# Performance work log

Measured on AMD Instinct MI355X. Metric: run time of the kernel, lower is better.

Reference implementation:

```python
import jax, jax.numpy as jnp
import numpy as np

B, L, E, H = 2, 2048, 1024, 16
HD = E // H


def _rel_shift(x):
    # x: [b, h, q, k] -> Transformer-XL relative shift via pad+reshape trick
    b, h, q, k = x.shape
    xp = jnp.pad(x, ((0, 0), (0, 0), (0, 0), (1, 0)))  # pad left of last dim
    xp = xp.reshape(b, h, k + 1, q)
    return xp[:, :, 1:, :].reshape(b, h, q, k)


def setup_inputs() -> dict:
    key = jax.random.key(0)
    ks = jax.random.split(key, 16)
    s = 0.02
    return {
        "query": jax.random.normal(ks[0], (B, L, E), jnp.float32),
        "key": jax.random.normal(ks[1], (B, L, E), jnp.float32),
        "value": jax.random.normal(ks[2], (B, L, E), jnp.float32),
        "pos_embedding": jax.random.normal(ks[3], (B, L, E), jnp.float32),
        "Wq": jax.random.normal(ks[4], (E, E), jnp.float32) * s,
        "bq": jnp.zeros((E,), jnp.float32),
        "Wk": jax.random.normal(ks[5], (E, E), jnp.float32) * s,
        "bk": jnp.zeros((E,), jnp.float32),
        "Wv": jax.random.normal(ks[6], (E, E), jnp.float32) * s,
        "bv": jnp.zeros((E,), jnp.float32),
        "Wp": jax.random.normal(ks[7], (E, E), jnp.float32) * s,  # Pos linear, no bias
        "Wo": jax.random.normal(ks[8], (E, E), jnp.float32) * s,
        "bo": jnp.zeros((E,), jnp.float32),
        "U": jax.random.normal(ks[9], (H, HD), jnp.float32) * s,
        "V": jax.random.normal(ks[10], (H, HD), jnp.float32) * s,
    }


def reference(query, key, value, pos_embedding, Wq, bq, Wk, bk, Wv, bv, Wp, Wo, bo, U, V):
    b, qlen, e = query.shape
    h, hd = U.shape
    scale = jnp.sqrt(jnp.asarray(e, query.dtype))
    # torch Linear: y = x @ W.T + b
    q = (query @ Wq.T + bq).reshape(b, qlen, h, hd)
    k = (key @ Wk.T + bk).reshape(b, key.shape[1], h, hd)
    v = (value @ Wv.T + bv).reshape(b, value.shape[1], h, hd)
    r = (pos_embedding @ Wp.T).reshape(b, -1, h, hd)
    content_score = jnp.einsum("bqhd,bkhd->bhqk", q + U, k)
    position_score = jnp.einsum("bqhd,bkhd->bhqk", q + V, r)
    position_score = _rel_shift(position_score)
    attention_score = (content_score + position_score) / scale
    # NOTE: the original module applies NO softmax; faithful reproduction.
    # einsum 'bhqk,bvhd->bqhd' sums over both k (scores) and v (values).
    alpha = jnp.einsum("bhqk,bvhd->bqhd", attention_score, v).reshape(b, qlen, e)
    return alpha @ Wo.T + bo
```

## Files before the change

### kernel.cpp

```cpp
#include <hip/hip_runtime.h>

#define BB 2
#define LL 2048
#define EE 1024
#define HH 16
#define HDD 64

typedef __bf16 bf16x8 __attribute__((ext_vector_type(8)));
typedef float f32x4 __attribute__((ext_vector_type(4)));

__device__ __forceinline__ unsigned short f2bf(float f) {
  unsigned int x = __float_as_uint(f);
  return (unsigned short)((x + 0x7FFFu + ((x >> 16) & 1u)) >> 16);
}

__global__ __launch_bounds__(256) void cast_kernel(
    const float* __restrict__ q, const float* __restrict__ pe,
    const float* __restrict__ wq, const float* __restrict__ wp,
    unsigned short* __restrict__ q16, unsigned short* __restrict__ pe16,
    unsigned short* __restrict__ wq16, unsigned short* __restrict__ wp16) {
  const int NQ4 = BB * LL * EE / 4;
  const int NW4 = EE * EE / 4;
  int i = blockIdx.x * 256 + threadIdx.x;
  const float* src; unsigned short* dst; int off;
  if (i < NQ4)                { src = q;  dst = q16;  off = i; }
  else if (i < 2 * NQ4)       { src = pe; dst = pe16; off = i - NQ4; }
  else if (i < 2 * NQ4 + NW4) { src = wq; dst = wq16; off = i - 2 * NQ4; }
  else                        { src = wp; dst = wp16; off = i - 2 * NQ4 - NW4; }
  float4 v = ((const float4*)src)[off];
  ushort4 u;
  u.x = f2bf(v.x); u.y = f2bf(v.y); u.z = f2bf(v.z); u.w = f2bf(v.w);
  ((ushort4*)dst)[off] = u;
}

__global__ __launch_bounds__(256) void sumkv_kernel(
    const float* __restrict__ key, const float* __restrict__ value,
    float* __restrict__ keysum, float* __restrict__ valsum) {
  int e = blockIdx.x * 256 + threadIdx.x;
  int b = blockIdx.z;
  int l0 = blockIdx.y * 64;
  size_t base = ((size_t)b * LL + l0) * EE + e;
  float ak = 0.f, av = 0.f;
  for (int i = 0; i < 64; i++) {
    ak += key[base + (size_t)i * EE];
    av += value[base + (size_t)i * EE];
  }
  atomicAdd(&keysum[b * EE + e], ak);
  atomicAdd(&valsum[b * EE + e], av);
}

__global__ __launch_bounds__(256) void proj_kernel(
    const float* __restrict__ keysum, const float* __restrict__ valsum,
    const float* __restrict__ Wk, const float* __restrict__ bk,
    const float* __restrict__ Wv, const float* __restrict__ bv,
    float* __restrict__ Kproj, float* __restrict__ Vproj) {
  int wv = threadIdx.x >> 6, lane = threadIdx.x & 63;
  int idx = blockIdx.x * 4 + wv;
  int b = idx >> 10, ep = idx & (EE - 1);
  const float* sum  = blockIdx.z ? valsum : keysum;
  const float* W    = blockIdx.z ? Wv : Wk;
  const float* bias = blockIdx.z ? bv : bk;
  float* outp       = blockIdx.z ? Vproj : Kproj;
  float acc = 0.f;
  for (int k = lane; k < EE; k += 64) acc += sum[b * EE + k] * W[ep * EE + k];
  for (int off = 32; off; off >>= 1) acc += __shfl_down(acc, off, 64);
  if (lane == 0) outp[b * EE + ep] = acc + (float)LL * bias[ep];
}

__global__ __launch_bounds__(256) void w2_kernel(
    const float* __restrict__ Vproj, const float* __restrict__ Wo,
    float* __restrict__ W2) {
  int wv = threadIdx.x >> 6, lane = threadIdx.x & 63;
  int idx = blockIdx.x * 4 + wv;
  int e = idx & (EE - 1);
  int h = (idx >> 10) & (HH - 1);
  int b = idx >> 14;
  float acc = Vproj[b * EE + h * HDD + lane] * Wo[(size_t)e * EE + h * HDD + lane];
  for (int off = 32; off; off >>= 1) acc += __shfl_down(acc, off, 64);
  if (lane == 0) W2[((size_t)b * HH + h) * EE + e] = acc;
}

__global__ __launch_bounds__(256) void gemm_kernel(
    const unsigned short* __restrict__ q16, const unsigned short* __restrict__ wq16,
    const float* __restrict__ bq, float* __restrict__ qout,
    const unsigned short* __restrict__ pe16, const unsigned short* __restrict__ wp16,
    float* __restrict__ rout) {
  const int K = EE, N = EE;
  const unsigned short* X; const unsigned short* W; const float* bias; float* Out;
  if (blockIdx.z == 0) { X = q16;  W = wq16; bias = bq;      Out = qout; }
  else                 { X = pe16; W = wp16; bias = nullptr; Out = rout; }

  __shared__ __align__(16) unsigned short As[128 * 32];
  __shared__ __align__(16) unsigned short Bs[128 * 32];

  const int tid = threadIdx.x;
  const int lane = tid & 63;
  const int wv = tid >> 6;
  const int wr = wv >> 1, wc = wv & 1;
  const int n0 = blockIdx.x * 128;
  const int m0 = blockIdx.y * 128;

  const int srow = tid >> 2;
  const int skc = (tid & 3) * 8;

  f32x4 acc[4][4];
#pragma unroll
  for (int i = 0; i < 4; i++)
#pragma unroll
    for (int j = 0; j < 4; j++) acc[i][j] = (f32x4)0.0f;

  const int arow = wr * 64 + (lane & 15);
  const int brow = wc * 64 + (lane & 15);
  const int koff = (lane >> 4) * 8;

  for (int kk = 0; kk < K; kk += 32) {
    *(uint4*)&As[srow * 32 + skc]        = *(const uint4*)&X[(size_t)(m0 + srow) * K + kk + skc];
    *(uint4*)&As[(srow + 64) * 32 + skc] = *(const uint4*)&X[(size_t)(m0 + srow + 64) * K + kk + skc];
    *(uint4*)&Bs[srow * 32 + skc]        = *(const uint4*)&W[(size_t)(n0 + srow) * K + kk + skc];
    *(uint4*)&Bs[(srow + 64) * 32 + skc] = *(const uint4*)&W[(size_t)(n0 + srow + 64) * K + kk + skc];
    __syncthreads();
    bf16x8 af[4], bf[4];
#pragma unroll
    for (int i = 0; i < 4; i++) af[i] = *(const bf16x8*)&As[(arow + i * 16) * 32 + koff];
#pragma unroll
    for (int j = 0; j < 4; j++) bf[j] = *(const bf16x8*)&Bs[(brow + j * 16) * 32 + koff];
#pragma unroll
    for (int i = 0; i < 4; i++)
#pragma unroll
      for (int j = 0; j < 4; j++)
        acc[i][j] = __builtin_amdgcn_mfma_f32_16x16x32_bf16(af[i], bf[j], acc[i][j], 0, 0, 0);
    __syncthreads();
  }

  const int rbase = m0 + wr * 64 + (lane >> 4) * 4;
  const int cbase = n0 + wc * 64 + (lane & 15);
#pragma unroll
  for (int i = 0; i < 4; i++) {
#pragma unroll
    for (int j = 0; j < 4; j++) {
      int col = cbase + j * 16;
      float badd = bias ? bias[col] : 0.f;
#pragma unroll
      for (int g = 0; g < 4; g++) {
        int row = rbase + i * 16 + g;
        Out[(size_t)row * N + col] = acc[i][j][g] + badd;
      }
    }
  }
}

__global__ __launch_bounds__(256) void scan1_kernel(
    const float* __restrict__ r, float* __restrict__ chunksum) {
  int e = blockIdx.x * 256 + threadIdx.x;
  int ch = blockIdx.y, b = blockIdx.z;
  size_t base = ((size_t)b * LL + ch * 64) * EE + e;
  float a = 0.f;
  for (int i = 0; i < 64; i++) a += r[base + (size_t)i * EE];
  chunksum[((size_t)b * 32 + ch) * EE + e] = a;
}

__global__ __launch_bounds__(256) void scan2_kernel(
    const float* __restrict__ r, const float* __restrict__ chunksum,
    float* __restrict__ P) {
  int e = blockIdx.x * 256 + threadIdx.x;
  int ch = blockIdx.y, b = blockIdx.z;
  float pre = 0.f;
  for (int c = 0; c < ch; c++) pre += chunksum[((size_t)b * 32 + c) * EE + e];
  size_t Pbase = (size_t)b * (LL + 1) * EE;
  if (ch == 0) P[Pbase + e] = 0.f;
  size_t rbase = ((size_t)b * LL + ch * 64) * EE + e;
  float run = pre;
  for (int i = 0; i < 64; i++) {
    run += r[rbase + (size_t)i * EE];
    P[Pbase + (size_t)(ch * 64 + i + 1) * EE + e] = run;
  }
}

__global__ __launch_bounds__(256) void score_kernel(
    const float* __restrict__ q, const float* __restrict__ P,
    const float* __restrict__ Kproj, const float* __restrict__ U,
    const float* __restrict__ V, float* __restrict__ S) {
  int wv = threadIdx.x >> 6, lane = threadIdx.x & 63;
  int g = blockIdx.x * 4 + wv;
  int b = g >> 11, p = g & (LL - 1);
  size_t qrow = (size_t)(b * LL + p) * EE;
  size_t Pbase = (size_t)b * (LL + 1) * EE;
  size_t prowL = Pbase + (size_t)LL * EE;
  size_t prowA = Pbase + (size_t)(LL - p - 1) * EE;
  bool hasB = (p < LL - 1);
  size_t prowB = hasB ? (Pbase + (size_t)(LL - p - 2) * EE) : Pbase;
  for (int h = 0; h < HH; h++) {
    int d = h * HDD + lane;
    float qd = q[qrow + d];
    float q2 = hasB ? q[qrow + EE + d] : 0.f;
    float kp = Kproj[b * EE + d];
    float pl = P[prowL + d];
    float pa = P[prowA + d];
    float pb = hasB ? P[prowB + d] : 0.f;
    float Uh = U[d], Vh = V[d];
    float t = (qd + Uh) * kp + (qd + Vh) * (pl - pa) + (q2 + Vh) * pb;
    for (int off = 32; off; off >>= 1) t += __shfl_down(t, off, 64);
    if (lane == 0) S[((size_t)b * HH + h) * LL + p] = t * (1.f / 32.f);
  }
}

__global__ __launch_bounds__(256) void out_kernel(
    const float* __restrict__ S, const float* __restrict__ W2,
    const float* __restrict__ bo, float* __restrict__ out) {
  int row = blockIdx.x;
  int b = row >> 11, p = row & (LL - 1);
  __shared__ float sh[HH];
  if (threadIdx.x < HH) sh[threadIdx.x] = S[((size_t)b * HH + threadIdx.x) * LL + p];
  __syncthreads();
  for (int e = threadIdx.x; e < EE; e += 256) {
    float acc = bo[e];
#pragma unroll
    for (int h = 0; h < HH; h++) acc += sh[h] * W2[((size_t)b * HH + h) * EE + e];
    out[(size_t)row * EE + e] = acc;
  }
}

extern "C" void kernel_launch(void* const* d_in, const int* in_sizes, int n_in,
                              void* d_out, int out_size, void* d_ws, size_t ws_size,
                              hipStream_t stream) {
  const float* query = (const float*)d_in[0];
  const float* key   = (const float*)d_in[1];
  const float* value = (const float*)d_in[2];
  const float* pos   = (const float*)d_in[3];
  const float* Wq = (const float*)d_in[4];
  const float* bq = (const float*)d_in[5];
  const float* Wk = (const float*)d_in[6];
  const float* bk = (const float*)d_in[7];
  const float* Wv = (const float*)d_in[8];
  const float* bv = (const float*)d_in[9];
  const float* Wp = (const float*)d_in[10];
  const float* Wo = (const float*)d_in[11];
  const float* bo = (const float*)d_in[12];
  const float* U  = (const float*)d_in[13];
  const float* V  = (const float*)d_in[14];
  float* out = (float*)d_out;

  char* ws = (char*)d_ws;
  size_t o = 0;
  auto take = [&](size_t bytes) -> char* {
    char* p = ws + o;
    o += (bytes + 255) & ~(size_t)255;
    return p;
  };
  float* keysum = (float*)take(BB * EE * 4);
  float* valsum = (float*)take(BB * EE * 4);
  float* Kproj  = (float*)take(BB * EE * 4);
  float* Vproj  = (float*)take(BB * EE * 4);
  float* W2     = (float*)take((size_t)BB * HH * EE * 4);
  float* S      = (float*)take((size_t)BB * HH * LL * 4);
  float* chunks = (float*)take((size_t)BB * 32 * EE * 4);
  float* qbuf   = (float*)take((size_t)BB * LL * EE * 4);
  float* rbuf   = (float*)take((size_t)BB * LL * EE * 4);
  float* Pbuf   = (float*)take((size_t)BB * (LL + 1) * EE * 4);
  unsigned short* q16  = (unsigned short*)take((size_t)BB * LL * EE * 2);
  unsigned short* pe16 = (unsigned short*)take((size_t)BB * LL * EE * 2);
  unsigned short* wq16 = (unsigned short*)take((size_t)EE * EE * 2);
  unsigned short* wp16 = (unsigned short*)take((size_t)EE * EE * 2);

  hipMemsetAsync(keysum, 0, (size_t)2 * BB * EE * 4, stream);

  cast_kernel<<<10240, 256, 0, stream>>>(query, pos, Wq, Wp, q16, pe16, wq16, wp16);
  sumkv_kernel<<<dim3(EE / 256, 32, BB), 256, 0, stream>>>(key, value, keysum, valsum);
  proj_kernel<<<dim3(BB * EE / 4, 1, 2), 256, 0, stream>>>(keysum, valsum, Wk, bk, Wv, bv, Kproj, Vproj);
  w2_kernel<<<dim3(BB * HH * EE / 4), 256, 0, stream>>>(Vproj, Wo, W2);
  gemm_kernel<<<dim3(EE / 128, BB * LL / 128, 2), 256, 0, stream>>>(q16, wq16, bq, qbuf, pe16, wp16, rbuf);
  scan1_kernel<<<dim3(EE / 256, 32, BB), 256, 0, stream>>>(rbuf, chunks);
  scan2_kernel<<<dim3(EE / 256, 32, BB), 256, 0, stream>>>(rbuf, chunks, Pbuf);
  score_kernel<<<dim3(BB * LL / 4), 256, 0, stream>>>(qbuf, Pbuf, Kproj, U, V, S);
  out_kernel<<<dim3(BB * LL), 256, 0, stream>>>(S, W2, bo, out);
}
```

Baseline: 249.0 us.

## Fuse cast and key/value sums, use direct-to-LDS loads, vectorize score and output

Merges the bf16 cast kernel and the key/value column-sum kernel into one launch and halves the sum chunk length to get more parallelism. The GEMM now stages tiles with global_load_lds, copying straight from global memory into shared memory without going through registers. The prefix-scan chunk count doubles. The score and output kernels switch to float4 loads and stores, and score uses a narrower shuffle reduction. Together these aim to cut launch overhead, register staging and scalar memory traffic, at the cost of more atomics and a GEMM LDS layout that depends on wave-ordered placement.

Result: no change. 252.6 us (+1.5%).

```diff
diff --git a/kernel.cpp b/kernel.cpp
--- a/kernel.cpp
+++ b/kernel.cpp
@@ -14,39 +14,47 @@
   return (unsigned short)((x + 0x7FFFu + ((x >> 16) & 1u)) >> 16);
 }
 
-__global__ __launch_bounds__(256) void cast_kernel(
+__device__ __forceinline__ void load_lds16(const void* g, void* l) {
+  __builtin_amdgcn_global_load_lds(
+      (const __attribute__((address_space(1))) void*)g,
+      (__attribute__((address_space(3))) void*)l, 16, 0, 0);
+}
+
+__global__ __launch_bounds__(256) void prelude_kernel(
     const float* __restrict__ q, const float* __restrict__ pe,
     const float* __restrict__ wq, const float* __restrict__ wp,
     unsigned short* __restrict__ q16, unsigned short* __restrict__ pe16,
-    unsigned short* __restrict__ wq16, unsigned short* __restrict__ wp16) {
-  const int NQ4 = BB * LL * EE / 4;
-  const int NW4 = EE * EE / 4;
-  int i = blockIdx.x * 256 + threadIdx.x;
-  const float* src; unsigned short* dst; int off;
-  if (i < NQ4)                { src = q;  dst = q16;  off = i; }
-  else if (i < 2 * NQ4)       { src = pe; dst = pe16; off = i - NQ4; }
-  else if (i < 2 * NQ4 + NW4) { src = wq; dst = wq16; off = i - 2 * NQ4; }
-  else                        { src = wp; dst = wp16; off = i - 2 * NQ4 - NW4; }
-  float4 v = ((const float4*)src)[off];
-  ushort4 u;
-  u.x = f2bf(v.x); u.y = f2bf(v.y); u.z = f2bf(v.z); u.w = f2bf(v.w);
-  ((ushort4*)dst)[off] = u;
-}
-
-__global__ __launch_bounds__(256) void sumkv_kernel(
+    unsigned short* __restrict__ wq16, unsigned short* __restrict__ wp16,
     const float* __restrict__ key, const float* __restrict__ value,
     float* __restrict__ keysum, float* __restrict__ valsum) {
-  int e = blockIdx.x * 256 + threadIdx.x;
-  int b = blockIdx.z;
-  int l0 = blockIdx.y * 64;
-  size_t base = ((size_t)b * LL + l0) * EE + e;
-  float ak = 0.f, av = 0.f;
-  for (int i = 0; i < 64; i++) {
-    ak += key[base + (size_t)i * EE];
-    av += value[base + (size_t)i * EE];
-  }
-  atomicAdd(&keysum[b * EE + e], ak);
-  atomicAdd(&valsum[b * EE + e], av);
+  if (blockIdx.x < 10240) {
+    const int NQ4 = BB * LL * EE / 4;
+    const int NW4 = EE * EE / 4;
+    int i = blockIdx.x * 256 + threadIdx.x;
+    const float* src; unsigned short* dst; int off;
+    if (i < NQ4)                { src = q;  dst = q16;  off = i; }
+    else if (i < 2 * NQ4)       { src = pe; dst = pe16; off = i - NQ4; }
+    else if (i < 2 * NQ4 + NW4) { src = wq; dst = wq16; off = i - 2 * NQ4; }
+    else                        { src = wp; dst = wp16; off = i - 2 * NQ4 - NW4; }
+    float4 v = ((const float4*)src)[off];
+    ushort4 u;
+    u.x = f2bf(v.x); u.y = f2bf(v.y); u.z = f2bf(v.z); u.w = f2bf(v.w);
+    ((ushort4*)dst)[off] = u;
+  } else {
+    int blk2 = blockIdx.x - 10240;
+    int b = blk2 >> 8;
+    int ch = (blk2 >> 2) & 63;
+    int es = blk2 & 3;
+    int e = es * 256 + threadIdx.x;
+    size_t base = ((size_t)b * LL + ch * 32) * EE + e;
+    float ak = 0.f, av = 0.f;
+    for (int i = 0; i < 32; i++) {
+      ak += key[base + (size_t)i * EE];
+      av += value[base + (size_t)i * EE];
+    }
+    atomicAdd(&keysum[b * EE + e], ak);
+    atomicAdd(&valsum[b * EE + e], av);
+  }
 }
 
 __global__ __launch_bounds__(256) void proj_kernel(
@@ -100,8 +108,12 @@
   const int n0 = blockIdx.x * 128;
   const int m0 = blockIdx.y * 128;
 
-  const int srow = tid >> 2;
-  const int skc = (tid & 3) * 8;
+  const int srow = wv * 16 + (lane >> 2);
+  const int scol = (lane & 3) * 8;
+  const unsigned short* gA = X + (size_t)(m0 + srow) * K + scol;
+  const unsigned short* gB = W + (size_t)(n0 + srow) * K + scol;
+  unsigned short* sA = As + wv * 512;
+  unsigned short* sB = Bs + wv * 512;
 
   f32x4 acc[4][4];
 #pragma unroll
@@ -114,10 +126,10 @@
   const int koff = (lane >> 4) * 8;
 
   for (int kk = 0; kk < K; kk += 32) {
-    *(uint4*)&As[srow * 32 + skc]        = *(const uint4*)&X[(size_t)(m0 + srow) * K + kk + skc];
-    *(uint4*)&As[(srow + 64) * 32 + skc] = *(const uint4*)&X[(size_t)(m0 + srow + 64) * K + kk + skc];
-    *(uint4*)&Bs[srow * 32 + skc]        = *(const uint4*)&W[(size_t)(n0 + srow) * K + kk + skc];
-    *(uint4*)&Bs[(srow + 64) * 32 + skc] = *(const uint4*)&W[(size_t)(n0 + srow + 64) * K + kk + skc];
+    load_lds16(gA + kk,                   sA);
+    load_lds16(gA + kk + (size_t)64 * K,  sA + 2048);
+    load_lds16(gB + kk,                   sB);
+    load_lds16(gB + kk + (size_t)64 * K,  sB + 2048);
     __syncthreads();
     bf16x8 af[4], bf[4];
 #pragma unroll
@@ -153,10 +165,10 @@
     const float* __restrict__ r, float* __restrict__ chunksum) {
   int e = blockIdx.x * 256 + threadIdx.x;
   int ch = blockIdx.y, b = blockIdx.z;
-  size_t base = ((size_t)b * LL + ch * 64) * EE + e;
+  size_t base = ((size_t)b * LL + ch * 32) * EE + e;
   float a = 0.f;
-  for (int i = 0; i < 64; i++) a += r[base + (size_t)i * EE];
-  chunksum[((size_t)b * 32 + ch) * EE + e] = a;
+  for (int i = 0; i < 32; i++) a += r[base + (size_t)i * EE];
+  chunksum[((size_t)b * 64 + ch) * EE + e] = a;
 }
 
 __global__ __launch_bounds__(256) void scan2_kernel(
@@ -165,14 +177,14 @@
   int e = blockIdx.x * 256 + threadIdx.x;
   int ch = blockIdx.y, b = blockIdx.z;
   float pre = 0.f;
-  for (int c = 0; c < ch; c++) pre += chunksum[((size_t)b * 32 + c) * EE + e];
+  for (int c = 0; c < ch; c++) pre += chunksum[((size_t)b * 64 + c) * EE + e];
   size_t Pbase = (size_t)b * (LL + 1) * EE;
   if (ch == 0) P[Pbase + e] = 0.f;
-  size_t rbase = ((size_t)b * LL + ch * 64) * EE + e;
+  size_t rbase = ((size_t)b * LL + ch * 32) * EE + e;
   float run = pre;
-  for (int i = 0; i < 64; i++) {
+  for (int i = 0; i < 32; i++) {
     run += r[rbase + (size_t)i * EE];
-    P[Pbase + (size_t)(ch * 64 + i + 1) * EE + e] = run;
+    P[Pbase + (size_t)(ch * 32 + i + 1) * EE + e] = run;
   }
 }
 
@@ -185,22 +197,35 @@
   int b = g >> 11, p = g & (LL - 1);
   size_t qrow = (size_t)(b * LL + p) * EE;
   size_t Pbase = (size_t)b * (LL + 1) * EE;
-  size_t prowL = Pbase + (size_t)LL * EE;
-  size_t prowA = Pbase + (size_t)(LL - p - 1) * EE;
   bool hasB = (p < LL - 1);
-  size_t prowB = hasB ? (Pbase + (size_t)(LL - p - 2) * EE) : Pbase;
-  for (int h = 0; h < HH; h++) {
-    int d = h * HDD + lane;
-    float qd = q[qrow + d];
-    float q2 = hasB ? q[qrow + EE + d] : 0.f;
-    float kp = Kproj[b * EE + d];
-    float pl = P[prowL + d];
-    float pa = P[prowA + d];
-    float pb = hasB ? P[prowB + d] : 0.f;
-    float Uh = U[d], Vh = V[d];
-    float t = (qd + Uh) * kp + (qd + Vh) * (pl - pa) + (q2 + Vh) * pb;
-    for (int off = 32; off; off >>= 1) t += __shfl_down(t, off, 64);
-    if (lane == 0) S[((size_t)b * HH + h) * LL + p] = t * (1.f / 32.f);
+  const float4* qv  = (const float4*)(q + qrow);
+  const float4* q2v = (const float4*)(q + qrow + EE);
+  const float4* PLv = (const float4*)(P + Pbase + (size_t)LL * EE);
+  const float4* PAv = (const float4*)(P + Pbase + (size_t)(LL - p - 1) * EE);
+  const float4* PBv = (const float4*)(P + Pbase + (size_t)(hasB ? (LL - p - 2) : 0) * EE);
+  const float4* KPv = (const float4*)(Kproj + b * EE);
+  const float4* Uv  = (const float4*)U;
+  const float4* Vv  = (const float4*)V;
+#pragma unroll
+  for (int it = 0; it < 4; it++) {
+    int idx = it * 64 + lane;
+    float4 qd = qv[idx];
+    float4 kp = KPv[idx], pl = PLv[idx], pa = PAv[idx];
+    float4 Uh = Uv[idx], Vh = Vv[idx];
+    float4 q2 = hasB ? q2v[idx] : make_float4(0.f, 0.f, 0.f, 0.f);
+    float4 pb = hasB ? PBv[idx] : make_float4(0.f, 0.f, 0.f, 0.f);
+    float t = (qd.x + Uh.x) * kp.x + (qd.x + Vh.x) * (pl.x - pa.x) + (q2.x + Vh.x) * pb.x
+            + (qd.y + Uh.y) * kp.y + (qd.y + Vh.y) * (pl.y - pa.y) + (q2.y + Vh.y) * pb.y
+            + (qd.z + Uh.z) * kp.z + (qd.z + Vh.z) * (pl.z - pa.z) + (q2.z + Vh.z) * pb.z
+            + (qd.w + Uh.w) * kp.w + (qd.w + Vh.w) * (pl.w - pa.w) + (q2.w + Vh.w) * pb.w;
+    t += __shfl_down(t, 8, 64);
+    t += __shfl_down(t, 4, 64);
+    t += __shfl_down(t, 2, 64);
+    t += __shfl_down(t, 1, 64);
+    if ((lane & 15) == 0) {
+      int h = it * 4 + (lane >> 4);
+      S[((size_t)b * HH + h) * LL + p] = t * (1.f / 32.f);
+    }
   }
 }
 
@@ -212,12 +237,16 @@
   __shared__ float sh[HH];
   if (threadIdx.x < HH) sh[threadIdx.x] = S[((size_t)b * HH + threadIdx.x) * LL + p];
   __syncthreads();
-  for (int e = threadIdx.x; e < EE; e += 256) {
-    float acc = bo[e];
-#pragma unroll
-    for (int h = 0; h < HH; h++) acc += sh[h] * W2[((size_t)b * HH + h) * EE + e];
-    out[(size_t)row * EE + e] = acc;
-  }
+  int e4 = threadIdx.x;
+  const float4* W2v = (const float4*)W2;
+  float4 acc = ((const float4*)bo)[e4];
+#pragma unroll
+  for (int h = 0; h < HH; h++) {
+    float s = sh[h];
+    float4 w = W2v[((size_t)b * HH + h) * 256 + e4];
+    acc.x += s * w.x; acc.y += s * w.y; acc.z += s * w.z; acc.w += s * w.w;
+  }
+  ((float4*)out)[(size_t)row * 256 + e4] = acc;
 }
 
 extern "C" void kernel_launch(void* const* d_in, const int* in_sizes, int n_in,
@@ -253,7 +282,7 @@
   float* Vproj  = (float*)take(BB * EE * 4);
   float* W2     = (float*)take((size_t)BB * HH * EE * 4);
   float* S      = (float*)take((size_t)BB * HH * LL * 4);
-  float* chunks = (float*)take((size_t)BB * 32 * EE * 4);
+  float* chunks = (float*)take((size_t)BB * 64 * EE * 4);
   float* qbuf   = (float*)take((size_t)BB * LL * EE * 4);
   float* rbuf   = (float*)take((size_t)BB * LL * EE * 4);
   float* Pbuf   = (float*)take((size_t)BB * (LL + 1) * EE * 4);
@@ -264,13 +293,13 @@
 
   hipMemsetAsync(keysum, 0, (size_t)2 * BB * EE * 4, stream);
 
-  cast_kernel<<<10240, 256, 0, stream>>>(query, pos, Wq, Wp, q16, pe16, wq16, wp16);
-  sumkv_kernel<<<dim3(EE / 256, 32, BB), 256, 0, stream>>>(key, value, keysum, valsum);
+  prelude_kernel<<<10752, 256, 0, stream>>>(query, pos, Wq, Wp, q16, pe16, wq16, wp16,
+                                            key, value, keysum, valsum);
   proj_kernel<<<dim3(BB * EE / 4, 1, 2), 256, 0, stream>>>(keysum, valsum, Wk, bk, Wv, bv, Kproj, Vproj);
   w2_kernel<<<dim3(BB * HH * EE / 4), 256, 0, stream>>>(Vproj, Wo, W2);
   gemm_kernel<<<dim3(EE / 128, BB * LL / 128, 2), 256, 0, stream>>>(q16, wq16, bq, qbuf, pe16, wp16, rbuf);
-  scan1_kernel<<<dim3(EE / 256, 32, BB), 256, 0, stream>>>(rbuf, chunks);
-  scan2_kernel<<<dim3(EE / 256, 32, BB), 256, 0, stream>>>(rbuf, chunks, Pbuf);
+  scan1_kernel<<<dim3(EE / 256, 64, BB), 256, 0, stream>>>(rbuf, chunks);
+  scan2_kernel<<<dim3(EE / 256, 64, BB), 256, 0, stream>>>(rbuf, chunks, Pbuf);
   score_kernel<<<dim3(BB * LL / 4), 256, 0, stream>>>(qbuf, Pbuf, Kproj, U, V, S);
   out_kernel<<<dim3(BB * LL), 256, 0, stream>>>(S, W2, bo, out);
 }
```
